# Performance work log

Measured on AMD Instinct MI355X. Metric: run time of the kernel, lower is better.

Reference implementation:

```python
import jax, jax.numpy as jnp
import numpy as np

SIZE = 1024
CODE_DIM = 256
B, H, W = 32, 32, 32


def setup_inputs() -> dict:
    key = jax.random.key(0)
    k1, k2 = jax.random.split(key)
    z = jax.random.normal(k1, (B, CODE_DIM, H, W), dtype=jnp.float32)
    embeddings = jax.random.normal(k2, (SIZE, CODE_DIM), dtype=jnp.float32)
    return {"z": z, "embeddings": embeddings}


def reference(z, embeddings):
    b, c, h, w = z.shape  # c == code_dim
    # (b, h, w, c) -> (N, c)
    flat = jnp.transpose(z, (0, 2, 3, 1)).reshape(-1, c)
    d = (
        jnp.sum(flat * flat, axis=-1, keepdims=True)
        - 2.0 * (flat @ embeddings.T)
        + jnp.sum(embeddings * embeddings, axis=-1)
    )
    idx = jnp.argmin(d, axis=-1)  # (N,)
    quantized = embeddings[idx].reshape(b, h, w, c)
    quantized = jnp.transpose(quantized, (0, 3, 1, 2))  # (b, c, h, w)
    straight_through = jax.lax.stop_gradient(quantized - z) + z
    return quantized, straight_through, idx.reshape(b, h, w)
```

## Files before the change

kernel.cpp:

```cpp
#include <hip/hip_runtime.h>

#define NPTS   32768
#define NCODES 1024
#define DIM    256
#define HWSZ   1024
#define CHW    (DIM*HWSZ)
#define QSZ    8388608

typedef __attribute__((ext_vector_type(8))) short short8;
typedef __attribute__((ext_vector_type(4))) float f32x4;

__device__ __forceinline__ unsigned bf16_rne(float f) {
    unsigned u = __float_as_uint(f);
    return (u + 0x7fffu + ((u >> 16) & 1u)) >> 16;
}

__device__ __forceinline__ unsigned long long pack_di(float d, int code) {
    unsigned u = __float_as_uint(d);
    unsigned key = u ^ ((unsigned)((int)u >> 31) | 0x80000000u);
    return ((unsigned long long)key << 32) | (unsigned)code;
}

__device__ __forceinline__ int fmoff(int n, int c) {
    return ((((((n >> 7) * 2 + ((n >> 6) & 1)) * 8 + (c >> 5)) * 4 + ((n >> 4) & 3)) * 4
             + ((c >> 3) & 3)) * 16 + (n & 15)) * 8 + (c & 7);
}

__global__ void k_prep(const float* __restrict__ z, const float* __restrict__ emb,
                       short* __restrict__ Xh, short* __restrict__ Xl,
                       short* __restrict__ Eh, short* __restrict__ El,
                       float* __restrict__ e2, unsigned long long* __restrict__ win) {
    int tid = threadIdx.x;
    if (blockIdx.x >= 2048) {
        int eb = blockIdx.x - 2048;
        int widx = eb * 256 + tid;
        if (widx < NPTS) win[widx] = ~0ull;
        int lane = tid & 63, w = tid >> 6;
        int k = eb * 4 + w;
        const float4 v = *reinterpret_cast<const float4*>(emb + k * DIM + lane * 4);
        float f[4] = {v.x, v.y, v.z, v.w};
        short h[4], l[4];
        double s = 0.0;
        #pragma unroll
        for (int i = 0; i < 4; ++i) {
            unsigned hb = bf16_rne(f[i]);
            float hf = __uint_as_float(hb << 16);
            h[i] = (short)hb;
            l[i] = (short)bf16_rne(f[i] - hf);
            s += (double)f[i] * f[i];
        }
        int eoff = fmoff(k, lane * 4);
        *reinterpret_cast<short4*>(Eh + eoff) = make_short4(h[0], h[1], h[2], h[3]);
        *reinterpret_cast<short4*>(El + eoff) = make_short4(l[0], l[1], l[2], l[3]);
        #pragma unroll
        for (int m = 32; m >= 1; m >>= 1) s += __shfl_xor(s, m);
        if (lane == 0) e2[k] = (float)s;
        return;
    }
    __shared__ float T[64][33];
    int blk = blockIdx.x;
    int b   = blk >> 6;
    int rem = blk & 63;
    int ht  = rem >> 1;
    int ch  = rem & 1;
    int hw0 = ht * 32;
    int n0  = b * HWSZ + hw0;
    int hq = tid & 7, cr = tid >> 3;
    int wp = tid >> 3, wc = tid & 7;
    const float* zp = z + b * CHW;
    #pragma unroll
    for (int cc2 = 0; cc2 < 2; ++cc2) {
        int c0 = (ch * 2 + cc2) * 64;
        if (cc2) __syncthreads();
        #pragma unroll
        for (int p = 0; p < 2; ++p) {
            int c = p * 32 + cr;
            float4 v = *reinterpret_cast<const float4*>(zp + (c0 + c) * HWSZ + hw0 + hq * 4);
            T[c][hq * 4 + 0] = v.x; T[c][hq * 4 + 1] = v.y;
            T[c][hq * 4 + 2] = v.z; T[c][hq * 4 + 3] = v.w;
        }
        __syncthreads();
        short8 hv, lv;
        #pragma unroll
        for (int k = 0; k < 8; ++k) {
            float f = T[wc * 8 + k][wp];
            unsigned hb = bf16_rne(f);
            float hf = __uint_as_float(hb << 16);
            hv[k] = (short)hb;
            lv[k] = (short)bf16_rne(f - hf);
        }
        int off = fmoff(n0 + wp, c0 + wc * 8);
        *reinterpret_cast<short8*>(Xh + off) = hv;
        *reinterpret_cast<short8*>(Xl + off) = lv;
    }
}

__launch_bounds__(256, 3)
__global__ void k_dist(const short* __restrict__ Xh, const short* __restrict__ Xl,
                       const short* __restrict__ Eh, const short* __restrict__ El,
                       const float* __restrict__ e2, unsigned long long* __restrict__ win) {
    __shared__ float sv[2][128];
    __shared__ int   si[2][128];

    const int tid = threadIdx.x;
    const int pt = blockIdx.x & 255;
    const int ct = blockIdx.x >> 8;
    const int n0 = pt * 128;
    const int c0 = ct * 128;

    const int w = tid >> 6, lane = tid & 63;
    const int wr = w >> 1, wc = w & 1;
    const int m16 = lane & 15, quad = lane >> 4;

    f32x4 acc[4][4];
    #pragma unroll
    for (int i = 0; i < 4; ++i)
        #pragma unroll
        for (int j = 0; j < 4; ++j) acc[i][j] = (f32x4){0.f, 0.f, 0.f, 0.f};

    const short* Ahb = Xh + (pt * 2 + wr) * 16384 + lane * 8;
    const short* Alb = Xl + (pt * 2 + wr) * 16384 + lane * 8;
    const short* Bhb = Eh + (ct * 2 + wc) * 16384 + lane * 8;
    const short* Blb = El + (ct * 2 + wc) * 16384 + lane * 8;

    for (int t = 0; t < 8; ++t) {
        const int to = t * 2048;
        short8 ah[4], al[4], bh[4], bl[4];
        #pragma unroll
        for (int i = 0; i < 4; ++i) {
            ah[i] = *reinterpret_cast<const short8*>(Ahb + to + i * 512);
            al[i] = *reinterpret_cast<const short8*>(Alb + to + i * 512);
        }
        #pragma unroll
        for (int j = 0; j < 4; ++j) {
            bh[j] = *reinterpret_cast<const short8*>(Bhb + to + j * 512);
            bl[j] = *reinterpret_cast<const short8*>(Blb + to + j * 512);
        }
        __builtin_amdgcn_s_setprio(1);
        #pragma unroll
        for (int i = 0; i < 4; ++i)
            #pragma unroll
            for (int j = 0; j < 4; ++j)
                acc[i][j] = __builtin_amdgcn_mfma_f32_16x16x32_bf16(ah[i], bh[j], acc[i][j], 0, 0, 0);
        #pragma unroll
        for (int i = 0; i < 4; ++i)
            #pragma unroll
            for (int j = 0; j < 4; ++j)
                acc[i][j] = __builtin_amdgcn_mfma_f32_16x16x32_bf16(al[i], bh[j], acc[i][j], 0, 0, 0);
        #pragma unroll
        for (int i = 0; i < 4; ++i)
            #pragma unroll
            for (int j = 0; j < 4; ++j)
                acc[i][j] = __builtin_amdgcn_mfma_f32_16x16x32_bf16(ah[i], bl[j], acc[i][j], 0, 0, 0);
        __builtin_amdgcn_s_setprio(0);
    }

    float ecol[4];
    #pragma unroll
    for (int j = 0; j < 4; ++j) ecol[j] = e2[c0 + wc * 64 + j * 16 + m16];

    #pragma unroll
    for (int i = 0; i < 4; ++i) {
        #pragma unroll
        for (int rr = 0; rr < 4; ++rr) {
            float best = 3.4e38f; int bi = 0;
            #pragma unroll
            for (int j = 0; j < 4; ++j) {
                float d = fmaf(-2.f, acc[i][j][rr], ecol[j]);
                int code = c0 + wc * 64 + j * 16 + m16;
                if (d < best) { best = d; bi = code; }
            }
            #pragma unroll
            for (int m = 1; m < 16; m <<= 1) {
                float ov = __shfl_xor(best, m);
                int   oi = __shfl_xor(bi, m);
                if (ov < best || (ov == best && oi < bi)) { best = ov; bi = oi; }
            }
            if (m16 == 0) {
                int p = wr * 64 + i * 16 + quad * 4 + rr;
                sv[wc][p] = best; si[wc][p] = bi;
            }
        }
    }
    __syncthreads();
    if (tid < 128) {
        float v0 = sv[0][tid]; int i0 = si[0][tid];
        float v1 = sv[1][tid]; int i1 = si[1][tid];
        if (v1 < v0) { v0 = v1; i0 = i1; }
        atomicMin(win + n0 + tid, pack_di(v0, i0));
    }
}

__global__ void k_out(const float* __restrict__ z, const float* __restrict__ emb,
                      const unsigned long long* __restrict__ win,
                      float* __restrict__ out) {
    __shared__ float Q[32][129];
    __shared__ int sbi[32];
    int blk = blockIdx.x;
    int n0 = (blk >> 1) * 32;
    int ch = blk & 1;
    int tid = threadIdx.x;
    if (tid < 32) {
        int n = n0 + tid;
        int bi = (int)(unsigned)(win[n] & 0xFFFFFFFFull);
        sbi[tid] = bi;
        if (ch == 0) out[2 * QSZ + n] = (float)bi;
    }
    __syncthreads();
    {
        int pt = tid >> 3, co = tid & 7;
        const float* ep = emb + sbi[pt] * DIM + ch * 128;
        #pragma unroll
        for (int j = 0; j < 4; ++j) {
            int c = j * 32 + co * 4;
            float4 v = *reinterpret_cast<const float4*>(ep + c);
            Q[pt][c] = v.x; Q[pt][c + 1] = v.y; Q[pt][c + 2] = v.z; Q[pt][c + 3] = v.w;
        }
    }
    __syncthreads();
    int hq = tid & 7, cr = tid >> 3;
    int b = n0 >> 10, hw0 = (n0 & 1023) + hq * 4;
    #pragma unroll
    for (int it = 0; it < 4; ++it) {
        int cl = it * 32 + cr;
        int c  = ch * 128 + cl;
        int off = b * CHW + c * HWSZ + hw0;
        float4 zv = *reinterpret_cast<const float4*>(z + off);
        float4 q = make_float4(Q[hq * 4 + 0][cl], Q[hq * 4 + 1][cl],
                               Q[hq * 4 + 2][cl], Q[hq * 4 + 3][cl]);
        *reinterpret_cast<float4*>(out + off) = q;
        float4 st = make_float4((q.x - zv.x) + zv.x, (q.y - zv.y) + zv.y,
                                (q.z - zv.z) + zv.z, (q.w - zv.w) + zv.w);
        *reinterpret_cast<float4*>(out + QSZ + off) = st;
    }
}

extern "C" void kernel_launch(void* const* d_in, const int* in_sizes, int n_in,
                              void* d_out, int out_size, void* d_ws, size_t ws_size,
                              hipStream_t stream) {
    const float* z   = (const float*)d_in[0];
    const float* emb = (const float*)d_in[1];
    float* out = (float*)d_out;
    float* ws  = (float*)d_ws;

    short* Eh   = (short*)ws;
    short* El   = (short*)(ws + 131072);
    float* e2   = ws + 262144;
    unsigned long long* win = (unsigned long long*)(ws + 263168);

    short* Xh = (short*)out;
    short* Xl = (short*)(out + 4194304);

    hipLaunchKernelGGL(k_prep, dim3(2304), dim3(256), 0, stream, z, emb, Xh, Xl, Eh, El, e2, win);
    hipLaunchKernelGGL(k_dist, dim3(2048), dim3(256), 0, stream, Xh, Xl, Eh, El, e2, win);
    hipLaunchKernelGGL(k_out,  dim3(2048), dim3(256), 0, stream, z, emb, win, out);
}
```

Baseline: 163.3 us.

## Stage codebook tiles through LDS with async global_load_lds double buffering

Codebook hi/lo fragments are now copied into a double-buffered shared-memory tile with direct global-to-LDS loads issued cooperatively by all four waves, so each fragment is fetched once per block rather than separately by each wave that uses it. The next tile's loads are prefetched while the current tile's MFMAs run, and the X-hi fragments are register double-buffered. Hand-placed waitcnt and barriers order the pipeline. In exchange the kernel uses 32KB more LDS and more registers, which may lower occupancy under the 3-blocks launch bound, and the manual vmcnt counting is fragile.

```diff
diff --git a/kernel.cpp b/kernel.cpp
--- a/kernel.cpp
+++ b/kernel.cpp
@@ -9,6 +9,12 @@
 
 typedef __attribute__((ext_vector_type(8))) short short8;
 typedef __attribute__((ext_vector_type(4))) float f32x4;
+
+__device__ __forceinline__ void gload16(const void* g, void* l) {
+    __builtin_amdgcn_global_load_lds((const __attribute__((address_space(1))) void*)g,
+                                     (__attribute__((address_space(3))) void*)l,
+                                     16, 0, 0);
+}
 
 __device__ __forceinline__ unsigned bf16_rne(float f) {
     unsigned u = __float_as_uint(f);
@@ -99,6 +105,7 @@
 __global__ void k_dist(const short* __restrict__ Xh, const short* __restrict__ Xl,
                        const short* __restrict__ Eh, const short* __restrict__ El,
                        const float* __restrict__ e2, unsigned long long* __restrict__ win) {
+    __shared__ __align__(16) short Bs[2][8192];
     __shared__ float sv[2][128];
     __shared__ int   si[2][128];
 
@@ -120,40 +127,67 @@
 
     const short* Ahb = Xh + (pt * 2 + wr) * 16384 + lane * 8;
     const short* Alb = Xl + (pt * 2 + wr) * 16384 + lane * 8;
-    const short* Bhb = Eh + (ct * 2 + wc) * 16384 + lane * 8;
-    const short* Blb = El + (ct * 2 + wc) * 16384 + lane * 8;
-
+    const short* Ebase = (w < 2 ? Eh : El) + (ct * 2 + wc) * 16384 + lane * 8;
+    char* BsW0 = (char*)&Bs[0][0] + w * 4096;
+    char* BsW1 = (char*)&Bs[1][0] + w * 4096;
+
+    #define STAGE_B(buf, tt) do {                                       \
+        char* d_ = (buf) ? BsW1 : BsW0;                                 \
+        const short* s_ = Ebase + (tt) * 2048;                          \
+        gload16(s_,        d_);                                         \
+        gload16(s_ + 512,  d_ + 1024);                                  \
+        gload16(s_ + 1024, d_ + 2048);                                  \
+        gload16(s_ + 1536, d_ + 3072);                                  \
+    } while (0)
+
+    short8 ah[2][4], al[4];
+    STAGE_B(0, 0);
+    #pragma unroll
+    for (int i = 0; i < 4; ++i)
+        ah[0][i] = *reinterpret_cast<const short8*>(Ahb + i * 512);
+
+    #pragma unroll
     for (int t = 0; t < 8; ++t) {
-        const int to = t * 2048;
-        short8 ah[4], al[4], bh[4], bl[4];
-        #pragma unroll
-        for (int i = 0; i < 4; ++i) {
-            ah[i] = *reinterpret_cast<const short8*>(Ahb + to + i * 512);
-            al[i] = *reinterpret_cast<const short8*>(Alb + to + i * 512);
-        }
-        #pragma unroll
-        for (int j = 0; j < 4; ++j) {
-            bh[j] = *reinterpret_cast<const short8*>(Bhb + to + j * 512);
-            bl[j] = *reinterpret_cast<const short8*>(Blb + to + j * 512);
-        }
-        __builtin_amdgcn_s_setprio(1);
+        const int cur = t & 1;
+        __builtin_amdgcn_s_barrier();
+        #pragma unroll
+        for (int i = 0; i < 4; ++i)
+            al[i] = *reinterpret_cast<const short8*>(Alb + t * 2048 + i * 512);
+        if (t < 7) STAGE_B(cur ^ 1, t + 1);
+        if (t < 7) asm volatile("s_waitcnt vmcnt(8)" ::: "memory");
+        else       asm volatile("s_waitcnt vmcnt(4)" ::: "memory");
+        __builtin_amdgcn_sched_barrier(0);
+
+        short8 bh[4];
+        #pragma unroll
+        for (int j = 0; j < 4; ++j)
+            bh[j] = *(const short8*)&Bs[cur][(wc * 4 + j) * 512 + lane * 8];
         #pragma unroll
         for (int i = 0; i < 4; ++i)
             #pragma unroll
             for (int j = 0; j < 4; ++j)
-                acc[i][j] = __builtin_amdgcn_mfma_f32_16x16x32_bf16(ah[i], bh[j], acc[i][j], 0, 0, 0);
+                acc[i][j] = __builtin_amdgcn_mfma_f32_16x16x32_bf16(ah[cur][i], bh[j], acc[i][j], 0, 0, 0);
         #pragma unroll
         for (int i = 0; i < 4; ++i)
             #pragma unroll
             for (int j = 0; j < 4; ++j)
                 acc[i][j] = __builtin_amdgcn_mfma_f32_16x16x32_bf16(al[i], bh[j], acc[i][j], 0, 0, 0);
+        if (t < 7) {
+            #pragma unroll
+            for (int i = 0; i < 4; ++i)
+                ah[cur ^ 1][i] = *reinterpret_cast<const short8*>(Ahb + (t + 1) * 2048 + i * 512);
+        }
+        short8 bl[4];
+        #pragma unroll
+        for (int j = 0; j < 4; ++j)
+            bl[j] = *(const short8*)&Bs[cur][(8 + wc * 4 + j) * 512 + lane * 8];
         #pragma unroll
         for (int i = 0; i < 4; ++i)
             #pragma unroll
             for (int j = 0; j < 4; ++j)
-                acc[i][j] = __builtin_amdgcn_mfma_f32_16x16x32_bf16(ah[i], bl[j], acc[i][j], 0, 0, 0);
-        __builtin_amdgcn_s_setprio(0);
-    }
+                acc[i][j] = __builtin_amdgcn_mfma_f32_16x16x32_bf16(ah[cur][i], bl[j], acc[i][j], 0, 0, 0);
+    }
+    #undef STAGE_B
 
     float ecol[4];
     #pragma unroll
```

New measurement: 165.8 us. No clear change (+1.6%).

## Fuse z conversion into distance kernel, iterate all codes per block in LDS

Applied to the files above, without the earlier changes.

The z-to-bf16 hi/lo split now happens inside the distance kernel and is staged into LDS instead of global scratch. Each block owns 128 points and loops over all 1024 codes with a running argmin, so the atomicMin and the win initialisation are replaced by a plain store. This removes the global round trip for the converted X and the atomics. The cost is a grid of only 256 blocks, each using about 128KB of LDS with launch bounds of 1, so occupancy and parallelism drop sharply and the conversion phase is serialized within each block.

```diff
diff --git a/kernel.cpp b/kernel.cpp
--- a/kernel.cpp
+++ b/kernel.cpp
@@ -26,159 +26,169 @@
              + ((c >> 3) & 3)) * 16 + (n & 15)) * 8 + (c & 7);
 }
 
-__global__ void k_prep(const float* __restrict__ z, const float* __restrict__ emb,
-                       short* __restrict__ Xh, short* __restrict__ Xl,
-                       short* __restrict__ Eh, short* __restrict__ El,
-                       float* __restrict__ e2, unsigned long long* __restrict__ win) {
+__global__ void k_emb(const float* __restrict__ emb,
+                      short* __restrict__ Eh, short* __restrict__ El,
+                      float* __restrict__ e2) {
     int tid = threadIdx.x;
-    if (blockIdx.x >= 2048) {
-        int eb = blockIdx.x - 2048;
-        int widx = eb * 256 + tid;
-        if (widx < NPTS) win[widx] = ~0ull;
-        int lane = tid & 63, w = tid >> 6;
-        int k = eb * 4 + w;
-        const float4 v = *reinterpret_cast<const float4*>(emb + k * DIM + lane * 4);
-        float f[4] = {v.x, v.y, v.z, v.w};
-        short h[4], l[4];
-        double s = 0.0;
-        #pragma unroll
-        for (int i = 0; i < 4; ++i) {
-            unsigned hb = bf16_rne(f[i]);
-            float hf = __uint_as_float(hb << 16);
-            h[i] = (short)hb;
-            l[i] = (short)bf16_rne(f[i] - hf);
-            s += (double)f[i] * f[i];
-        }
-        int eoff = fmoff(k, lane * 4);
-        *reinterpret_cast<short4*>(Eh + eoff) = make_short4(h[0], h[1], h[2], h[3]);
-        *reinterpret_cast<short4*>(El + eoff) = make_short4(l[0], l[1], l[2], l[3]);
-        #pragma unroll
-        for (int m = 32; m >= 1; m >>= 1) s += __shfl_xor(s, m);
-        if (lane == 0) e2[k] = (float)s;
-        return;
-    }
+    int lane = tid & 63, w = tid >> 6;
+    int k = blockIdx.x * 4 + w;
+    const float4 v = *reinterpret_cast<const float4*>(emb + k * DIM + lane * 4);
+    float f[4] = {v.x, v.y, v.z, v.w};
+    short h[4], l[4];
+    double s = 0.0;
+    #pragma unroll
+    for (int i = 0; i < 4; ++i) {
+        unsigned hb = bf16_rne(f[i]);
+        float hf = __uint_as_float(hb << 16);
+        h[i] = (short)hb;
+        l[i] = (short)bf16_rne(f[i] - hf);
+        s += (double)f[i] * f[i];
+    }
+    int eoff = fmoff(k, lane * 4);
+    *reinterpret_cast<short4*>(Eh + eoff) = make_short4(h[0], h[1], h[2], h[3]);
+    *reinterpret_cast<short4*>(El + eoff) = make_short4(l[0], l[1], l[2], l[3]);
+    #pragma unroll
+    for (int m = 32; m >= 1; m >>= 1) s += __shfl_xor(s, m);
+    if (lane == 0) e2[k] = (float)s;
+}
+
+__launch_bounds__(256, 1)
+__global__ void k_main(const float* __restrict__ z,
+                       const short* __restrict__ Eh, const short* __restrict__ El,
+                       const float* __restrict__ e2,
+                       unsigned long long* __restrict__ win) {
+    __shared__ __align__(16) short Ah_lds[32768];
+    __shared__ __align__(16) short Al_lds[32768];
     __shared__ float T[64][33];
-    int blk = blockIdx.x;
-    int b   = blk >> 6;
-    int rem = blk & 63;
-    int ht  = rem >> 1;
-    int ch  = rem & 1;
-    int hw0 = ht * 32;
-    int n0  = b * HWSZ + hw0;
-    int hq = tid & 7, cr = tid >> 3;
-    int wp = tid >> 3, wc = tid & 7;
-    const float* zp = z + b * CHW;
-    #pragma unroll
-    for (int cc2 = 0; cc2 < 2; ++cc2) {
-        int c0 = (ch * 2 + cc2) * 64;
-        if (cc2) __syncthreads();
-        #pragma unroll
-        for (int p = 0; p < 2; ++p) {
-            int c = p * 32 + cr;
-            float4 v = *reinterpret_cast<const float4*>(zp + (c0 + c) * HWSZ + hw0 + hq * 4);
-            T[c][hq * 4 + 0] = v.x; T[c][hq * 4 + 1] = v.y;
-            T[c][hq * 4 + 2] = v.z; T[c][hq * 4 + 3] = v.w;
-        }
-        __syncthreads();
-        short8 hv, lv;
-        #pragma unroll
-        for (int k = 0; k < 8; ++k) {
-            float f = T[wc * 8 + k][wp];
-            unsigned hb = bf16_rne(f);
-            float hf = __uint_as_float(hb << 16);
-            hv[k] = (short)hb;
-            lv[k] = (short)bf16_rne(f - hf);
-        }
-        int off = fmoff(n0 + wp, c0 + wc * 8);
-        *reinterpret_cast<short8*>(Xh + off) = hv;
-        *reinterpret_cast<short8*>(Xl + off) = lv;
-    }
-}
-
-__launch_bounds__(256, 3)
-__global__ void k_dist(const short* __restrict__ Xh, const short* __restrict__ Xl,
-                       const short* __restrict__ Eh, const short* __restrict__ El,
-                       const float* __restrict__ e2, unsigned long long* __restrict__ win) {
     __shared__ float sv[2][128];
     __shared__ int   si[2][128];
 
     const int tid = threadIdx.x;
-    const int pt = blockIdx.x & 255;
-    const int ct = blockIdx.x >> 8;
-    const int n0 = pt * 128;
-    const int c0 = ct * 128;
+    const int n0 = blockIdx.x * 128;
+    const int b = n0 >> 10, hw0 = n0 & 1023;
+
+    {
+        int hq = tid & 7, cr = tid >> 3;
+        int wp = tid >> 3, wcc = tid & 7;
+        const float* zp = z + b * CHW;
+        for (int ht = 0; ht < 4; ++ht) {
+            int hwb = hw0 + ht * 32;
+            for (int cc = 0; cc < 4; ++cc) {
+                int c0 = cc * 64;
+                __syncthreads();
+                #pragma unroll
+                for (int p = 0; p < 2; ++p) {
+                    int c = p * 32 + cr;
+                    float4 v = *reinterpret_cast<const float4*>(zp + (c0 + c) * HWSZ + hwb + hq * 4);
+                    T[c][hq * 4 + 0] = v.x; T[c][hq * 4 + 1] = v.y;
+                    T[c][hq * 4 + 2] = v.z; T[c][hq * 4 + 3] = v.w;
+                }
+                __syncthreads();
+                short8 hv, lv;
+                #pragma unroll
+                for (int k = 0; k < 8; ++k) {
+                    float f = T[wcc * 8 + k][wp];
+                    unsigned hb = bf16_rne(f);
+                    float hf = __uint_as_float(hb << 16);
+                    hv[k] = (short)hb;
+                    lv[k] = (short)bf16_rne(f - hf);
+                }
+                int off = fmoff(ht * 32 + wp, c0 + wcc * 8);
+                *reinterpret_cast<short8*>(&Ah_lds[off]) = hv;
+                *reinterpret_cast<short8*>(&Al_lds[off]) = lv;
+            }
+        }
+    }
+    __syncthreads();
 
     const int w = tid >> 6, lane = tid & 63;
     const int wr = w >> 1, wc = w & 1;
     const int m16 = lane & 15, quad = lane >> 4;
 
-    f32x4 acc[4][4];
+    const short* AhL = Ah_lds + wr * 16384 + lane * 8;
+    const short* AlL = Al_lds + wr * 16384 + lane * 8;
+
+    float best[4][4]; int bidx[4][4];
     #pragma unroll
     for (int i = 0; i < 4; ++i)
         #pragma unroll
-        for (int j = 0; j < 4; ++j) acc[i][j] = (f32x4){0.f, 0.f, 0.f, 0.f};
-
-    const short* Ahb = Xh + (pt * 2 + wr) * 16384 + lane * 8;
-    const short* Alb = Xl + (pt * 2 + wr) * 16384 + lane * 8;
-    const short* Bhb = Eh + (ct * 2 + wc) * 16384 + lane * 8;
-    const short* Blb = El + (ct * 2 + wc) * 16384 + lane * 8;
-
-    for (int t = 0; t < 8; ++t) {
-        const int to = t * 2048;
-        short8 ah[4], al[4], bh[4], bl[4];
-        #pragma unroll
-        for (int i = 0; i < 4; ++i) {
-            ah[i] = *reinterpret_cast<const short8*>(Ahb + to + i * 512);
-            al[i] = *reinterpret_cast<const short8*>(Alb + to + i * 512);
-        }
-        #pragma unroll
-        for (int j = 0; j < 4; ++j) {
-            bh[j] = *reinterpret_cast<const short8*>(Bhb + to + j * 512);
-            bl[j] = *reinterpret_cast<const short8*>(Blb + to + j * 512);
-        }
-        __builtin_amdgcn_s_setprio(1);
+        for (int rr = 0; rr < 4; ++rr) { best[i][rr] = 3.4e38f; bidx[i][rr] = 0; }
+
+    for (int ct = 0; ct < 8; ++ct) {
+        const short* Bhb = Eh + (ct * 2 + wc) * 16384 + lane * 8;
+        const short* Blb = El + (ct * 2 + wc) * 16384 + lane * 8;
+
+        f32x4 acc[4][4];
         #pragma unroll
         for (int i = 0; i < 4; ++i)
             #pragma unroll
-            for (int j = 0; j < 4; ++j)
-                acc[i][j] = __builtin_amdgcn_mfma_f32_16x16x32_bf16(ah[i], bh[j], acc[i][j], 0, 0, 0);
+            for (int j = 0; j < 4; ++j) acc[i][j] = (f32x4){0.f, 0.f, 0.f, 0.f};
+
+        #pragma unroll
+        for (int t = 0; t < 8; ++t) {
+            const int to = t * 2048;
+            short8 ah[4], al[4], bh[4], bl[4];
+            #pragma unroll
+            for (int i = 0; i < 4; ++i) {
+                ah[i] = *reinterpret_cast<const short8*>(AhL + to + i * 512);
+                al[i] = *reinterpret_cast<const short8*>(AlL + to + i * 512);
+            }
+            #pragma unroll
+            for (int j = 0; j < 4; ++j) {
+                bh[j] = *reinterpret_cast<const short8*>(Bhb + to + j * 512);
+                bl[j] = *reinterpret_cast<const short8*>(Blb + to + j * 512);
+            }
+            __builtin_amdgcn_s_setprio(1);
+            #pragma unroll
+            for (int i = 0; i < 4; ++i)
+                #pragma unroll
+                for (int j = 0; j < 4; ++j)
+                    acc[i][j] = __builtin_amdgcn_mfma_f32_16x16x32_bf16(ah[i], bh[j], acc[i][j], 0, 0, 0);
+            #pragma unroll
+            for (int i = 0; i < 4; ++i)
+                #pragma unroll
+                for (int j = 0; j < 4; ++j)
+                    acc[i][j] = __builtin_amdgcn_mfma_f32_16x16x32_bf16(al[i], bh[j], acc[i][j], 0, 0, 0);
+            #pragma unroll
+            for (int i = 0; i < 4; ++i)
+                #pragma unroll
+                for (int j = 0; j < 4; ++j)
+                    acc[i][j] = __builtin_amdgcn_mfma_f32_16x16x32_bf16(ah[i], bl[j], acc[i][j], 0, 0, 0);
+            __builtin_amdgcn_s_setprio(0);
+        }
+
+        const int c0 = ct * 128;
+        float e0[4];
+        #pragma unroll
+        for (int j = 0; j < 4; ++j) e0[j] = e2[c0 + wc * 64 + j * 16 + m16];
         #pragma unroll
         for (int i = 0; i < 4; ++i)
             #pragma unroll
-            for (int j = 0; j < 4; ++j)
-                acc[i][j] = __builtin_amdgcn_mfma_f32_16x16x32_bf16(al[i], bh[j], acc[i][j], 0, 0, 0);
-        #pragma unroll
-        for (int i = 0; i < 4; ++i)
-            #pragma unroll
-            for (int j = 0; j < 4; ++j)
-                acc[i][j] = __builtin_amdgcn_mfma_f32_16x16x32_bf16(ah[i], bl[j], acc[i][j], 0, 0, 0);
-        __builtin_amdgcn_s_setprio(0);
-    }
-
-    float ecol[4];
-    #pragma unroll
-    for (int j = 0; j < 4; ++j) ecol[j] = e2[c0 + wc * 64 + j * 16 + m16];
+            for (int rr = 0; rr < 4; ++rr)
+                #pragma unroll
+                for (int j = 0; j < 4; ++j) {
+                    float d = fmaf(-2.f, acc[i][j][rr], e0[j]);
+                    if (d < best[i][rr]) {
+                        best[i][rr] = d;
+                        bidx[i][rr] = c0 + wc * 64 + j * 16 + m16;
+                    }
+                }
+    }
 
     #pragma unroll
     for (int i = 0; i < 4; ++i) {
         #pragma unroll
         for (int rr = 0; rr < 4; ++rr) {
-            float best = 3.4e38f; int bi = 0;
-            #pragma unroll
-            for (int j = 0; j < 4; ++j) {
-                float d = fmaf(-2.f, acc[i][j][rr], ecol[j]);
-                int code = c0 + wc * 64 + j * 16 + m16;
-                if (d < best) { best = d; bi = code; }
-            }
+            float bv = best[i][rr]; int bi = bidx[i][rr];
             #pragma unroll
             for (int m = 1; m < 16; m <<= 1) {
-                float ov = __shfl_xor(best, m);
+                float ov = __shfl_xor(bv, m);
                 int   oi = __shfl_xor(bi, m);
-                if (ov < best || (ov == best && oi < bi)) { best = ov; bi = oi; }
+                if (ov < bv || (ov == bv && oi < bi)) { bv = ov; bi = oi; }
             }
             if (m16 == 0) {
                 int p = wr * 64 + i * 16 + quad * 4 + rr;
-                sv[wc][p] = best; si[wc][p] = bi;
+                sv[wc][p] = bv; si[wc][p] = bi;
             }
         }
     }
@@ -186,8 +196,8 @@
     if (tid < 128) {
         float v0 = sv[0][tid]; int i0 = si[0][tid];
         float v1 = sv[1][tid]; int i1 = si[1][tid];
-        if (v1 < v0) { v0 = v1; i0 = i1; }
-        atomicMin(win + n0 + tid, pack_di(v0, i0));
+        if (v1 < v0 || (v1 == v0 && i1 < i0)) { v0 = v1; i0 = i1; }
+        win[n0 + tid] = pack_di(v0, i0);
     }
 }
 
@@ -248,10 +258,7 @@
     float* e2   = ws + 262144;
     unsigned long long* win = (unsigned long long*)(ws + 263168);
 
-    short* Xh = (short*)out;
-    short* Xl = (short*)(out + 4194304);
-
-    hipLaunchKernelGGL(k_prep, dim3(2304), dim3(256), 0, stream, z, emb, Xh, Xl, Eh, El, e2, win);
-    hipLaunchKernelGGL(k_dist, dim3(2048), dim3(256), 0, stream, Xh, Xl, Eh, El, e2, win);
+    hipLaunchKernelGGL(k_emb,  dim3(256),  dim3(256), 0, stream, emb, Eh, El, e2);
+    hipLaunchKernelGGL(k_main, dim3(256),  dim3(256), 0, stream, z, Eh, El, e2, win);
     hipLaunchKernelGGL(k_out,  dim3(2048), dim3(256), 0, stream, z, emb, win, out);
 }
```

Measured after the change: 162.2 us. No clear change (-0.7%).
